# Kernel tuning notes

Measured on AMD Instinct MI355X. Metric: run time of the kernel, lower is better.

Reference implementation:

```python
import jax, jax.numpy as jnp
import numpy as np

NUM_COMPONENTS = 32
RESOLUTION = 512
NUM_POINTS = 2_000_000


def setup_inputs() -> dict:
    key = jax.random.key(0)
    kp, k0, k1, k2 = jax.random.split(key, 4)
    # positions are grid_sample-style normalized coords in [-1, 1]
    positions = jax.random.uniform(kp, (NUM_POINTS, 3), jnp.float32, -1.0, 1.0)
    vec_x = jax.random.normal(k0, (NUM_COMPONENTS, RESOLUTION), jnp.float32)
    vec_y = jax.random.normal(k1, (NUM_COMPONENTS, RESOLUTION), jnp.float32)
    vec_z = jax.random.normal(k2, (NUM_COMPONENTS, RESOLUTION), jnp.float32)
    return {"positions": positions, "vec_x": vec_x, "vec_y": vec_y, "vec_z": vec_z}


def _sample_1d(vec, x):
    """1D bilinear lookup mimicking grid_sample(align_corners=True, padding='zeros').
    vec: [C, R] per-axis CP vectors; x: [N] coords in [-1, 1]. Returns [C, N]."""
    R = vec.shape[1]
    ix = (x + 1.0) * 0.5 * (R - 1)          # map [-1,1] -> [0, R-1]
    i0 = jnp.floor(ix)
    w1 = ix - i0                              # right-neighbor weight
    i0i = i0.astype(jnp.int32)
    i1i = i0i + 1

    def gather(idx):
        valid = (idx >= 0) & (idx < R)        # zero-padding outside the grid
        g = jnp.take(vec, jnp.clip(idx, 0, R - 1), axis=1)  # [C, N]
        return jnp.where(valid[None, :], g, 0.0)

    return gather(i0i) * (1.0 - w1)[None, :] + gather(i1i) * w1[None, :]


def reference(positions, vec_x, vec_y, vec_z):
    # positions: [..., 3]; unbind per axis, 1D-sample each CP vector set, product-reduce.
    batch_shape = positions.shape[:-1]
    flat = positions.reshape(-1, 3)
    fx = _sample_1d(vec_x, flat[:, 0])  # [C, N]
    fy = _sample_1d(vec_y, flat[:, 1])  # [C, N]
    fz = _sample_1d(vec_z, flat[:, 2])  # [C, N]
    feats = fx * fy * fz                 # elementwise product over axes, [C, N]
    return feats.T.reshape(*batch_shape, vec_x.shape[0])  # [..., C]
```

## Files before the change

kernel.cpp:

```cpp
#include <hip/hip_runtime.h>

#define NC 32
#define NR 512

__global__ __launch_bounds__(256) void transpose_vecs(
    const float* __restrict__ vx, const float* __restrict__ vy,
    const float* __restrict__ vz, float* __restrict__ tx,
    float* __restrict__ ty, float* __restrict__ tz) {
  int u = blockIdx.x * 256 + threadIdx.x;
  if (u >= 3 * NC * NR) return;
  int table = u >> 14;
  int e = u & (NC * NR - 1);
  int c = e >> 9;
  int r = e & (NR - 1);
  const float* src = (table == 0) ? vx : (table == 1) ? vy : vz;
  float* dst = (table == 0) ? tx : (table == 1) ? ty : tz;
  dst[r * NC + c] = src[e];
}

__device__ __forceinline__ float4 sample4_t(const float* __restrict__ t,
                                            float x, int c4) {
  float ix = (x + 1.0f) * 0.5f * (float)(NR - 1);
  float f = floorf(ix);
  float w = ix - f;
  int i0 = (int)f;
  int i1 = i0 + 1;
  float m0 = (i0 >= 0 && i0 < NR) ? (1.0f - w) : 0.0f;
  float m1 = (i1 >= 0 && i1 < NR) ? w : 0.0f;
  int ci0 = min(max(i0, 0), NR - 1);
  int ci1 = min(max(i1, 0), NR - 1);
  float4 v0 = *(const float4*)(t + ci0 * NC + c4);
  float4 v1 = *(const float4*)(t + ci1 * NC + c4);
  float4 r;
  r.x = v0.x * m0 + v1.x * m1;
  r.y = v0.y * m0 + v1.y * m1;
  r.z = v0.z * m0 + v1.z * m1;
  r.w = v0.w * m0 + v1.w * m1;
  return r;
}

__device__ __forceinline__ float4 sample4_u(const float* __restrict__ t,
                                            float x, int c4) {
  float ix = (x + 1.0f) * 0.5f * (float)(NR - 1);
  float f = floorf(ix);
  float w = ix - f;
  int i0 = (int)f;
  int i1 = i0 + 1;
  float m0 = (i0 >= 0 && i0 < NR) ? (1.0f - w) : 0.0f;
  float m1 = (i1 >= 0 && i1 < NR) ? w : 0.0f;
  int ci0 = min(max(i0, 0), NR - 1);
  int ci1 = min(max(i1, 0), NR - 1);
  float4 r;
  float* rp = (float*)&r;
  for (int j = 0; j < 4; ++j) {
    float v0 = t[(c4 + j) * NR + ci0];
    float v1 = t[(c4 + j) * NR + ci1];
    rp[j] = v0 * m0 + v1 * m1;
  }
  return r;
}

template <bool TRANSPOSED>
__global__ __launch_bounds__(256) void cp_encode(
    const float* __restrict__ pos, const float* __restrict__ tx,
    const float* __restrict__ ty, const float* __restrict__ tz,
    float* __restrict__ out, int npts) {
  int t = blockIdx.x * 256 + threadIdx.x;
  int p = t >> 3;
  if (p >= npts) return;
  int c4 = (t & 7) * 4;

  float x = pos[3 * p + 0];
  float y = pos[3 * p + 1];
  float z = pos[3 * p + 2];

  float4 fx, fy, fz;
  if (TRANSPOSED) {
    fx = sample4_t(tx, x, c4);
    fy = sample4_t(ty, y, c4);
    fz = sample4_t(tz, z, c4);
  } else {
    fx = sample4_u(tx, x, c4);
    fy = sample4_u(ty, y, c4);
    fz = sample4_u(tz, z, c4);
  }

  float4 r;
  r.x = fx.x * fy.x * fz.x;
  r.y = fx.y * fy.y * fz.y;
  r.z = fx.z * fy.z * fz.z;
  r.w = fx.w * fy.w * fz.w;
  *(float4*)(out + (long long)p * NC + c4) = r;
}

extern "C" void kernel_launch(void* const* d_in, const int* in_sizes, int n_in,
                              void* d_out, int out_size, void* d_ws,
                              size_t ws_size, hipStream_t stream) {
  const float* pos = (const float*)d_in[0];
  const float* vx = (const float*)d_in[1];
  const float* vy = (const float*)d_in[2];
  const float* vz = (const float*)d_in[3];
  float* out = (float*)d_out;
  int npts = in_sizes[0] / 3;

  const size_t tbytes = (size_t)3 * NC * NR * sizeof(float);
  int total_threads = npts * 8;
  int blocks = (total_threads + 255) / 256;

  if (ws_size >= tbytes) {
    float* tx = (float*)d_ws;
    float* ty = tx + NC * NR;
    float* tz = ty + NC * NR;
    int tb = (3 * NC * NR + 255) / 256;
    transpose_vecs<<<tb, 256, 0, stream>>>(vx, vy, vz, tx, ty, tz);
    cp_encode<true><<<blocks, 256, 0, stream>>>(pos, tx, ty, tz, out, npts);
  } else {
    cp_encode<false><<<blocks, 256, 0, stream>>>(pos, vx, vy, vz, out, npts);
  }
}
```

Baseline: 314.6 us.

## Process four points per thread with vector position loads and nontemporal stores

Each thread now handles four points for its channel slice, loading positions as three float4 values and issuing all table gathers before interpolating, to raise memory-level parallelism. Output is written with nontemporal stores to avoid polluting caches with the large streaming result. The untransposed fallback path is removed, so the workspace is now assumed to be large enough. Register pressure rises and the grid becomes four times smaller.

```diff
diff --git a/kernel.cpp b/kernel.cpp
--- a/kernel.cpp
+++ b/kernel.cpp
@@ -2,6 +2,8 @@
 
 #define NC 32
 #define NR 512
+
+typedef float nf4 __attribute__((ext_vector_type(4)));
 
 __global__ __launch_bounds__(256) void transpose_vecs(
     const float* __restrict__ vx, const float* __restrict__ vy,
@@ -18,79 +20,96 @@
   dst[r * NC + c] = src[e];
 }
 
-__device__ __forceinline__ float4 sample4_t(const float* __restrict__ t,
-                                            float x, int c4) {
+struct Samp {
+  int o0, o1;
+  float m0, m1;
+};
+
+__device__ __forceinline__ Samp prep(float x) {
   float ix = (x + 1.0f) * 0.5f * (float)(NR - 1);
   float f = floorf(ix);
   float w = ix - f;
   int i0 = (int)f;
   int i1 = i0 + 1;
-  float m0 = (i0 >= 0 && i0 < NR) ? (1.0f - w) : 0.0f;
-  float m1 = (i1 >= 0 && i1 < NR) ? w : 0.0f;
-  int ci0 = min(max(i0, 0), NR - 1);
-  int ci1 = min(max(i1, 0), NR - 1);
-  float4 v0 = *(const float4*)(t + ci0 * NC + c4);
-  float4 v1 = *(const float4*)(t + ci1 * NC + c4);
+  Samp s;
+  s.m0 = (i0 >= 0 && i0 < NR) ? (1.0f - w) : 0.0f;
+  s.m1 = (i1 >= 0 && i1 < NR) ? w : 0.0f;
+  s.o0 = min(max(i0, 0), NR - 1) * NC;
+  s.o1 = min(max(i1, 0), NR - 1) * NC;
+  return s;
+}
+
+__device__ __forceinline__ float4 lerp4(float4 a, float4 b, float m0, float m1) {
   float4 r;
-  r.x = v0.x * m0 + v1.x * m1;
-  r.y = v0.y * m0 + v1.y * m1;
-  r.z = v0.z * m0 + v1.z * m1;
-  r.w = v0.w * m0 + v1.w * m1;
+  r.x = a.x * m0 + b.x * m1;
+  r.y = a.y * m0 + b.y * m1;
+  r.z = a.z * m0 + b.z * m1;
+  r.w = a.w * m0 + b.w * m1;
   return r;
 }
 
-__device__ __forceinline__ float4 sample4_u(const float* __restrict__ t,
-                                            float x, int c4) {
-  float ix = (x + 1.0f) * 0.5f * (float)(NR - 1);
-  float f = floorf(ix);
-  float w = ix - f;
-  int i0 = (int)f;
-  int i1 = i0 + 1;
-  float m0 = (i0 >= 0 && i0 < NR) ? (1.0f - w) : 0.0f;
-  float m1 = (i1 >= 0 && i1 < NR) ? w : 0.0f;
-  int ci0 = min(max(i0, 0), NR - 1);
-  int ci1 = min(max(i1, 0), NR - 1);
-  float4 r;
-  float* rp = (float*)&r;
-  for (int j = 0; j < 4; ++j) {
-    float v0 = t[(c4 + j) * NR + ci0];
-    float v1 = t[(c4 + j) * NR + ci1];
-    rp[j] = v0 * m0 + v1 * m1;
-  }
-  return r;
-}
-
-template <bool TRANSPOSED>
-__global__ __launch_bounds__(256) void cp_encode(
+__global__ __launch_bounds__(256) void cp_encode4(
     const float* __restrict__ pos, const float* __restrict__ tx,
     const float* __restrict__ ty, const float* __restrict__ tz,
     float* __restrict__ out, int npts) {
   int t = blockIdx.x * 256 + threadIdx.x;
-  int p = t >> 3;
-  if (p >= npts) return;
+  int pg = t >> 3;
   int c4 = (t & 7) * 4;
+  int p0 = pg * 4;
+  if (p0 >= npts) return;
 
-  float x = pos[3 * p + 0];
-  float y = pos[3 * p + 1];
-  float z = pos[3 * p + 2];
-
-  float4 fx, fy, fz;
-  if (TRANSPOSED) {
-    fx = sample4_t(tx, x, c4);
-    fy = sample4_t(ty, y, c4);
-    fz = sample4_t(tz, z, c4);
+  float px[4], py[4], pz[4];
+  if (p0 + 4 <= npts) {
+    const float4* pv = (const float4*)(pos + (size_t)p0 * 3);
+    float4 a = pv[0], b = pv[1], c = pv[2];
+    px[0] = a.x; py[0] = a.y; pz[0] = a.z;
+    px[1] = a.w; py[1] = b.x; pz[1] = b.y;
+    px[2] = b.z; py[2] = b.w; pz[2] = c.x;
+    px[3] = c.y; py[3] = c.z; pz[3] = c.w;
   } else {
-    fx = sample4_u(tx, x, c4);
-    fy = sample4_u(ty, y, c4);
-    fz = sample4_u(tz, z, c4);
+#pragma unroll
+    for (int j = 0; j < 4; ++j) {
+      int p = min(p0 + j, npts - 1);
+      px[j] = pos[3 * p + 0];
+      py[j] = pos[3 * p + 1];
+      pz[j] = pos[3 * p + 2];
+    }
   }
 
-  float4 r;
-  r.x = fx.x * fy.x * fz.x;
-  r.y = fx.y * fy.y * fz.y;
-  r.z = fx.z * fy.z * fz.z;
-  r.w = fx.w * fy.w * fz.w;
-  *(float4*)(out + (long long)p * NC + c4) = r;
+  Samp sx[4], sy[4], sz[4];
+#pragma unroll
+  for (int j = 0; j < 4; ++j) {
+    sx[j] = prep(px[j]);
+    sy[j] = prep(py[j]);
+    sz[j] = prep(pz[j]);
+  }
+
+  float4 vx0[4], vx1[4], vy0[4], vy1[4], vz0[4], vz1[4];
+#pragma unroll
+  for (int j = 0; j < 4; ++j) {
+    vx0[j] = *(const float4*)(tx + sx[j].o0 + c4);
+    vx1[j] = *(const float4*)(tx + sx[j].o1 + c4);
+    vy0[j] = *(const float4*)(ty + sy[j].o0 + c4);
+    vy1[j] = *(const float4*)(ty + sy[j].o1 + c4);
+    vz0[j] = *(const float4*)(tz + sz[j].o0 + c4);
+    vz1[j] = *(const float4*)(tz + sz[j].o1 + c4);
+  }
+
+#pragma unroll
+  for (int j = 0; j < 4; ++j) {
+    int p = p0 + j;
+    if (p < npts) {
+      float4 fx = lerp4(vx0[j], vx1[j], sx[j].m0, sx[j].m1);
+      float4 fy = lerp4(vy0[j], vy1[j], sy[j].m0, sy[j].m1);
+      float4 fz = lerp4(vz0[j], vz1[j], sz[j].m0, sz[j].m1);
+      nf4 r;
+      r.x = fx.x * fy.x * fz.x;
+      r.y = fx.y * fy.y * fz.y;
+      r.z = fx.z * fy.z * fz.z;
+      r.w = fx.w * fy.w * fz.w;
+      __builtin_nontemporal_store(r, (nf4*)(out + (size_t)p * NC + c4));
+    }
+  }
 }
 
 extern "C" void kernel_launch(void* const* d_in, const int* in_sizes, int n_in,
@@ -103,18 +122,14 @@
   float* out = (float*)d_out;
   int npts = in_sizes[0] / 3;
 
-  const size_t tbytes = (size_t)3 * NC * NR * sizeof(float);
-  int total_threads = npts * 8;
+  float* tx = (float*)d_ws;
+  float* ty = tx + NC * NR;
+  float* tz = ty + NC * NR;
+  int tb = (3 * NC * NR + 255) / 256;
+  transpose_vecs<<<tb, 256, 0, stream>>>(vx, vy, vz, tx, ty, tz);
+
+  int pgroups = (npts + 3) / 4;
+  int total_threads = pgroups * 8;
   int blocks = (total_threads + 255) / 256;
-
-  if (ws_size >= tbytes) {
-    float* tx = (float*)d_ws;
-    float* ty = tx + NC * NR;
-    float* tz = ty + NC * NR;
-    int tb = (3 * NC * NR + 255) / 256;
-    transpose_vecs<<<tb, 256, 0, stream>>>(vx, vy, vz, tx, ty, tz);
-    cp_encode<true><<<blocks, 256, 0, stream>>>(pos, tx, ty, tz, out, npts);
-  } else {
-    cp_encode<false><<<blocks, 256, 0, stream>>>(pos, vx, vy, vz, out, npts);
-  }
+  cp_encode4<<<blocks, 256, 0, stream>>>(pos, tx, ty, tz, out, npts);
 }
```

After: 329.6 us. 4.8% more time.
